# Performance work log

Measured on AMD Instinct MI355X. Metric: run time of the kernel, lower is better.

## Reference

```python
import jax, jax.numpy as jnp
import numpy as np

NEG_INF = -1e9
B, Q, M, D, H = 8, 512, 512, 1024, 16
S = D // H  # size per head


def rel_shift(x):
    # x: [B, H, Q, R] -> TransformerXL relative shift
    b, h, q, r = x.shape
    x = jnp.pad(x, ((0, 0), (0, 0), (0, 0), (1, 0)))
    x = x.reshape(b, h, r + 1, q)[:, :, 1:, :]
    return x.reshape(b, h, q, r)


def setup_inputs() -> dict:
    key = jax.random.key(0)
    ks = jax.random.split(key, 10)
    query_seqs = jax.random.normal(ks[0], (B, Q, D), jnp.float32)
    memory_seqs = jax.random.normal(ks[1], (B, M, D), jnp.float32)
    positional_encoding = jax.random.normal(ks[2], (Q + M, D), jnp.float32)
    # causal mask over concatenated [memory | query]: query token i may attend
    # to all memory tokens and query tokens <= i. 1 = masked.
    q_idx = jnp.arange(Q)[:, None]
    r_idx = jnp.arange(Q + M)[None, :]
    token_mask = (r_idx > q_idx + M).astype(jnp.float32)[None, None]  # [1,1,Q,Q+M]
    std = 0.02
    Wq = jax.random.normal(ks[3], (D, H, S), jnp.float32) * std
    Wk = jax.random.normal(ks[4], (D, H, S), jnp.float32) * std
    Wv = jax.random.normal(ks[5], (D, H, S), jnp.float32) * std
    Wr = jax.random.normal(ks[6], (D, H, S), jnp.float32) * std
    Wo = jax.random.normal(ks[7], (H, S, D), jnp.float32) * std
    content_bias = jax.random.normal(ks[8], (H, S), jnp.float32) * std
    position_bias = jax.random.normal(ks[9], (H, S), jnp.float32) * std
    return dict(query_seqs=query_seqs, memory_seqs=memory_seqs,
                positional_encoding=positional_encoding, token_mask=token_mask,
                Wq=Wq, Wk=Wk, Wv=Wv, Wr=Wr, Wo=Wo,
                content_bias=content_bias, position_bias=position_bias)


def reference(query_seqs, memory_seqs, positional_encoding, token_mask,
              Wq, Wk, Wv, Wr, Wo, content_bias, position_bias):
    # reference = [memory | query] along time axis
    reference_seqs = jnp.concatenate([memory_seqs, query_seqs], axis=1)  # [B,R,D]
    q = jnp.einsum('bqd,dhs->bqhs', query_seqs, Wq)       # [B,Q,H,S]
    k = jnp.einsum('brd,dhs->brhs', reference_seqs, Wk)   # [B,R,H,S]
    v = jnp.einsum('brd,dhs->brhs', reference_seqs, Wv)   # [B,R,H,S]
    r = jnp.einsum('rd,dhs->rhs', positional_encoding, Wr)  # [R,H,S]

    content = jnp.einsum('bqhs,brhs->bhqr', q + content_bias, k)
    positions = jnp.einsum('bqhs,rhs->bhqr', q + position_bias, r)
    positions = rel_shift(positions)

    logits = (content + positions) / jnp.sqrt(jnp.float32(S))
    logits = logits + token_mask * NEG_INF
    attn = jax.nn.softmax(logits, axis=3)  # dropout disabled (inference)

    out = jnp.einsum('bhqr,brhs->bqhs', attn, v)
    return jnp.einsum('bqhs,hsd->bqd', out, Wo)
```

## Files before the change

### kernel.cpp

```cpp
#include <hip/hip_runtime.h>

typedef _Float16 f16;
typedef _Float16 f16x8 __attribute__((ext_vector_type(8)));
typedef float f32x4 __attribute__((ext_vector_type(4)));

#define MFMA_F16(a, b, c) __builtin_amdgcn_mfma_f32_16x16x32_f16((a), (b), (c), 0, 0, 0)

#define SCL 0.125f

__device__ __forceinline__ void gl_lds16(const void* g, void* l) {
    __builtin_amdgcn_global_load_lds((const __attribute__((address_space(1))) unsigned int*)g,
                                     (__attribute__((address_space(3))) unsigned int*)l, 16, 0, 0);
}

__global__ void prep(const float* __restrict__ q, const float* __restrict__ mem,
                     const float* __restrict__ Wq, const float* __restrict__ Wk,
                     const float* __restrict__ Wv, const float* __restrict__ Wr,
                     const float* __restrict__ Wo,
                     f16* __restrict__ wt, f16* __restrict__ ref16)
{
    __shared__ float t[32][33];
    const int bid = blockIdx.x, tid = threadIdx.x;
    if (bid < 5120) {
        const int wi = bid >> 10, tt = bid & 1023;
        const float* src;
        switch (wi) { case 0: src = Wq; break; case 1: src = Wk; break;
                      case 2: src = Wv; break; case 3: src = Wr; break; default: src = Wo; }
        f16* dst = wt + ((size_t)wi << 20);
        const int x = (tt & 31) * 32, y = (tt >> 5) * 32;
        const int tx = tid & 31, ty = tid >> 5;
#pragma unroll
        for (int k2 = 0; k2 < 4; ++k2)
            t[ty + k2 * 8][tx] = src[(size_t)(y + ty + k2 * 8) * 1024 + x + tx];
        __syncthreads();
#pragma unroll
        for (int k2 = 0; k2 < 4; ++k2)
            dst[(size_t)(x + ty + k2 * 8) * 1024 + y + tx] = (f16)t[tx][ty + k2 * 8];
    } else {
        const int idx = (bid - 5120) * 256 + tid;
        const int half = idx >> 19;
        const int c = idx & 0x7FFFF;
        const int b = c >> 16, i = (c >> 7) & 511, ch = c & 127;
        const float* src = (half == 0 ? q : mem) + (((size_t)(b * 512 + i)) << 10) + ch * 8;
        const int t2 = (half == 0) ? (512 + i) : i;
        f16* dst = ref16 + ((((size_t)b << 10) + t2) << 10) + ch * 8;
        const float4 f0 = reinterpret_cast<const float4*>(src)[0];
        const float4 f1 = reinterpret_cast<const float4*>(src)[1];
        f16x8 v;
        v[0] = (f16)f0.x; v[1] = (f16)f0.y; v[2] = (f16)f0.z; v[3] = (f16)f0.w;
        v[4] = (f16)f1.x; v[5] = (f16)f1.y; v[6] = (f16)f1.z; v[7] = (f16)f1.w;
        *reinterpret_cast<f16x8*>(dst) = v;
    }
}

__global__ __launch_bounds__(512, 4)
void proj_kernel(const f16* __restrict__ ref16, const float* __restrict__ posenc,
                 const f16* __restrict__ wts,
                 f16* __restrict__ qc16, f16* __restrict__ qp16,
                 f16* __restrict__ k16, f16* __restrict__ vT16, f16* __restrict__ r16,
                 const float* __restrict__ cb, const float* __restrict__ pbias)
{
    __shared__ __align__(16) f16 SH[24576];
    f16* At = SH;
    f16* Bt = SH + 8192;

    const int tid = threadIdx.x, lane = tid & 63, w = tid >> 6;
    const int wr = w >> 2, wc = w & 3;

    const int bid = blockIdx.x;
    int mode, local, perx, shf;
    if (bid < 128)       { mode = 0; local = bid;        perx = 4; shf = 2; }
    else if (bid < 384)  { mode = 1; local = bid - 128;  perx = 8; shf = 3; }
    else if (bid < 640)  { mode = 2; local = bid - 384;  perx = 8; shf = 3; }
    else                 { mode = 3; local = bid - 640;  perx = 1; shf = 0; }
    const int xcd = local & 7, m = local >> 3;
    const int rt = xcd * perx + (m & (perx - 1));
    const int ct = m >> shf;
    const int i0 = rt * 128, n0 = ct * 256;
    const f16* BT = wts + ((size_t)mode << 20);

    f32x4 acc[4][4] = {};

    for (int ks = 0; ks < 16; ++ks) {
        const int k0 = ks * 64;
#pragma unroll
        for (int it = 0; it < 2; ++it) {
            const int c = tid + it * 512;
            const int row = c >> 3, ch = c & 7, chs = ch ^ (row & 7);
            const int grow = i0 + row;
            char* lA = reinterpret_cast<char*>(At) + ((c & ~63) << 4);
            if (mode == 3) {
                const float* sr = posenc + (size_t)grow * 1024 + k0 + ch * 8;
                const float4 f0 = reinterpret_cast<const float4*>(sr)[0];
                const float4 f1 = reinterpret_cast<const float4*>(sr)[1];
                f16x8 av;
                av[0] = (f16)f0.x; av[1] = (f16)f0.y; av[2] = (f16)f0.z; av[3] = (f16)f0.w;
                av[4] = (f16)f1.x; av[5] = (f16)f1.y; av[6] = (f16)f1.z; av[7] = (f16)f1.w;
                *reinterpret_cast<f16x8*>(reinterpret_cast<char*>(At) + row * 128 + (chs << 4)) = av;
            } else {
                const size_t arow = (mode == 0) ? (size_t)((grow >> 9) * 1024 + 512 + (grow & 511))
                                                : (size_t)grow;
                gl_lds16(ref16 + arow * 1024 + k0 + chs * 8, lA);
            }
        }
#pragma unroll
        for (int it = 0; it < 4; ++it) {
            const int c = tid + it * 512;
            const int row = c >> 3, ch = c & 7, chs = ch ^ (row & 7);
            char* lB = reinterpret_cast<char*>(Bt) + ((c & ~63) << 4);
            gl_lds16(BT + (size_t)(n0 + row) * 1024 + k0 + chs * 8, lB);
        }
        __syncthreads();
#pragma unroll
        for (int kk = 0; kk < 2; ++kk) {
            f16x8 avf[4], bvf[4];
            const int chh = kk * 4 + (lane >> 4);
#pragma unroll
            for (int mi = 0; mi < 4; ++mi) {
                const int row = wr * 64 + mi * 16 + (lane & 15);
                avf[mi] = *reinterpret_cast<const f16x8*>(reinterpret_cast<char*>(At) + row * 128 + ((chh ^ (row & 7)) << 4));
            }
#pragma unroll
            for (int n = 0; n < 4; ++n) {
                const int row = wc * 64 + n * 16 + (lane & 15);
                bvf[n] = *reinterpret_cast<const f16x8*>(reinterpret_cast<char*>(Bt) + row * 128 + ((chh ^ (row & 7)) << 4));
            }
#pragma unroll
            for (int mi = 0; mi < 4; ++mi)
#pragma unroll
                for (int n = 0; n < 4; ++n)
                    acc[mi][n] = MFMA_F16(avf[mi], bvf[n], acc[mi][n]);
        }
        __syncthreads();
    }

    if (mode == 2) {
#pragma unroll
        for (int hf = 0; hf < 2; ++hf) {
            if ((wc >> 1) == hf) {
#pragma unroll
                for (int mi = 0; mi < 4; ++mi)
#pragma unroll
                    for (int n = 0; n < 4; ++n)
#pragma unroll
                        for (int rg = 0; rg < 4; ++rg) {
                            const int jl = wr * 64 + mi * 16 + (lane >> 4) * 4 + rg;
                            const int cl = (wc & 1) * 64 + n * 16 + (lane & 15);
                            SH[cl * 128 + jl] = (f16)acc[mi][n][rg];
                        }
            }
            __syncthreads();
            const int b = i0 >> 10;
            const int j0l = i0 & 1023;
#pragma unroll
            for (int it = 0; it < 4; ++it) {
                const int c = tid + it * 512;
                const int cl = c >> 4, ch = c & 15;
                const int col = n0 + hf * 128 + cl;
                const int h = col >> 6, s = col & 63;
                f16* dst = vT16 + (((size_t)(b * 16 + h) * 64 + s) * 1024 + j0l + ch * 8);
                *reinterpret_cast<f16x8*>(dst) = *reinterpret_cast<const f16x8*>(SH + cl * 128 + ch * 8);
            }
            __syncthreads();
        }
    } else {
#pragma unroll
        for (int mi = 0; mi < 4; ++mi)
#pragma unroll
            for (int n = 0; n < 4; ++n)
#pragma unroll
                for (int rg = 0; rg < 4; ++rg) {
                    const int row = i0 + wr * 64 + mi * 16 + (lane >> 4) * 4 + rg;
                    const int col = n0 + wc * 64 + n * 16 + (lane & 15);
                    const float v = acc[mi][n][rg];
                    if (mode == 0) {
                        const int b = row >> 9, i = row & 511, h = col >> 6, s = col & 63;
                        const size_t idx = (((size_t)(b * 16 + h) * 512) + i) * 64 + s;
                        qc16[idx] = (f16)((v + cb[col]) * SCL);
                        qp16[idx] = (f16)((v + pbias[col]) * SCL);
                    } else if (mode == 1) {
                        const int b = row >> 10, j = row & 1023, h = col >> 6, s = col & 63;
                        k16[(((size_t)(b * 16 + h) * 1024) + j) * 64 + s] = (f16)v;
                    } else {
                        const int h = col >> 6, s = col & 63;
                        r16[((size_t)h * 1024 + row) * 64 + s] = (f16)v;
                    }
                }
    }
}

__global__ __launch_bounds__(512, 4)
void oproj_kernel(const f16* __restrict__ ao16, const f16* __restrict__ WoT, float* __restrict__ out)
{
    __shared__ __align__(16) f16 SH[24576];
    f16* At = SH;
    f16* Bt = SH + 8192;
    const int tid = threadIdx.x, lane = tid & 63, w = tid >> 6;
    const int wr = w >> 2, wc = w & 3;
    const int xcd = blockIdx.x & 7, m = blockIdx.x >> 3;
    const int rt = xcd * 4 + (m & 3), ct = m >> 2;
    const int i0 = rt * 128, n0 = ct * 256;

    f32x4 acc[4][4] = {};
    for (int ks = 0; ks < 16; ++ks) {
        const int k0 = ks * 64;
#pragma unroll
        for (int it = 0; it < 2; ++it) {
            const int c = tid + it * 512;
            const int row = c >> 3, ch = c & 7, chs = ch ^ (row & 7);
            gl_lds16(ao16 + (size_t)(i0 + row) * 1024 + k0 + chs * 8,
                     reinterpret_cast<char*>(At) + ((c & ~63) << 4));
        }
#pragma unroll
        for (int it = 0; it < 4; ++it) {
            const int c = tid + it * 512;
            const int row = c >> 3, ch = c & 7, chs = ch ^ (row & 7);
            gl_lds16(WoT + (size_t)(n0 + row) * 1024 + k0 + chs * 8,
                     reinterpret_cast<char*>(Bt) + ((c & ~63) << 4));
        }
        __syncthreads();
#pragma unroll
        for (int kk = 0; kk < 2; ++kk) {
            f16x8 avf[4], bvf[4];
            const int chh = kk * 4 + (lane >> 4);
#pragma unroll
            for (int mi = 0; mi < 4; ++mi) {
                const int row = wr * 64 + mi * 16 + (lane & 15);
                avf[mi] = *reinterpret_cast<const f16x8*>(reinterpret_cast<char*>(At) + row * 128 + ((chh ^ (row & 7)) << 4));
            }
#pragma unroll
            for (int n = 0; n < 4; ++n) {
                const int row = wc * 64 + n * 16 + (lane & 15);
                bvf[n] = *reinterpret_cast<const f16x8*>(reinterpret_cast<char*>(Bt) + row * 128 + ((chh ^ (row & 7)) << 4));
            }
#pragma unroll
            for (int mi = 0; mi < 4; ++mi)
#pragma unroll
                for (int n = 0; n < 4; ++n)
                    acc[mi][n] = MFMA_F16(avf[mi], bvf[n], acc[mi][n]);
        }
        __syncthreads();
    }
#pragma unroll
    for (int mi = 0; mi < 4; ++mi)
#pragma unroll
        for (int n = 0; n < 4; ++n)
#pragma unroll
            for (int rg = 0; rg < 4; ++rg) {
                const int row = i0 + wr * 64 + mi * 16 + (lane >> 4) * 4 + rg;
                const int col = n0 + wc * 64 + n * 16 + (lane & 15);
                out[(size_t)row * 1024 + col] = acc[mi][n][rg];
            }
}

__global__ __launch_bounds__(512, 4)
void attn_kernel(const f16* __restrict__ qc16, const f16* __restrict__ qp16,
                 const f16* __restrict__ k16, const f16* __restrict__ vT16,
                 const f16* __restrict__ r16, f16* __restrict__ attnout)
{
    __shared__ __align__(16) f16 KT[4096], VT[4096], RT[4096];
    __shared__ __align__(16) f16 PR[128 * 68];
    __shared__ __align__(16) f16 PB[8 * 2 * 16 * 68];

    const int tid = threadIdx.x, lane = tid & 63, w = tid >> 6;
    const int n = blockIdx.x;
    const int xcd = n & 7, m = n >> 3;
    const int h = xcd + 8 * (m >> 5);
    const int b = (m >> 2) & 7;
    const int iB = m & 3;
    const int i0 = iB * 128;
    const int bh = b * 16 + h;

    const f16* kbase = k16 + (size_t)bh * 1024 * 64;
    const f16* vbase = vT16 + (size_t)bh * 64 * 1024;
    const f16* rbase = r16 + (size_t)h * 1024 * 64;

    f16x8 qcf[2], qpf[2];
    {
        const size_t qoff = ((size_t)bh * 512 + i0 + w * 16 + (lane & 15)) * 64;
#pragma unroll
        for (int kk = 0; kk < 2; ++kk) {
            const int ch = (kk * 4 + (lane >> 4)) * 8;
            qcf[kk] = *reinterpret_cast<const f16x8*>(qc16 + qoff + ch);
            qpf[kk] = *reinterpret_cast<const f16x8*>(qp16 + qoff + ch);
        }
    }

    auto stage64 = [&](f16* dst, const f16* src, int rowstride) {
        const int row = tid >> 3, ch = tid & 7, chs = ch ^ (row & 7);
        gl_lds16(src + (size_t)row * rowstride + chs * 8,
                 reinterpret_cast<char*>(dst) + ((tid & ~63) << 4));
    };

    auto compute_pblock = [&](int bt) {
        const int slot = bt & 1;
        f32x4 pc[4] = {};
#pragma unroll
        for (int kk = 0; kk < 2; ++kk) {
            const int chh = kk * 4 + (lane >> 4);
#pragma unroll
            for (int tf = 0; tf < 4; ++tf) {
                const int brow = tf * 16 + (lane & 15);
                const f16x8 rv = *reinterpret_cast<const f16x8*>(reinterpret_cast<char*>(RT) + brow * 128 + ((chh ^ (brow & 7)) << 4));
                pc[tf] = MFMA_F16(qpf[kk], rv, pc[tf]);
            }
        }
        f16* pbw = PB + (size_t)((w * 2 + slot) * 16) * 68;
#pragma unroll
        for (int tf = 0; tf < 4; ++tf)
#pragma unroll
            for (int rg = 0; rg < 4; ++rg) {
                const int r = (lane >> 4) * 4 + rg;
                pbw[r * 68 + tf * 16 + (lane & 15)] = (f16)pc[tf][rg];
            }
    };

    {
        const int bt0 = 6 - 2 * iB;
        stage64(RT, rbase + (size_t)(bt0 * 64) * 64, 64);
        __syncthreads();
        compute_pblock(bt0);
        __syncthreads();
        stage64(RT, rbase + (size_t)((bt0 + 1) * 64) * 64, 64);
        __syncthreads();
        compute_pblock(bt0 + 1);
    }

    float mrun[4] = {-1e30f, -1e30f, -1e30f, -1e30f};
    float lrun[4] = {0.f, 0.f, 0.f, 0.f};
    f32x4 o[4] = {};

    const int njt = 2 * iB + 10;
    for (int jt = 0; jt < njt; ++jt) {
        const int j0 = jt * 64;
        const int bt = jt - 2 * iB + 8;
        __syncthreads();
        stage64(KT, kbase + (size_t)j0 * 64, 64);
        stage64(VT, vbase + j0, 1024);
        if (bt <= 15) stage64(RT, rbase + (size_t)(bt * 64) * 64, 64);
        __syncthreads();

        if (w < 4 && bt <= 15) compute_pblock(bt);

        f32x4 cfr[4] = {};
        __builtin_amdgcn_s_setprio(1);
#pragma unroll
        for (int kk = 0; kk < 2; ++kk) {
            const int chh = kk * 4 + (lane >> 4);
#pragma unroll
            for (int jf = 0; jf < 4; ++jf) {
                const int brow = jf * 16 + (lane & 15);
                const f16x8 kv = *reinterpret_cast<const f16x8*>(reinterpret_cast<char*>(KT) + brow * 128 + ((chh ^ (brow & 7)) << 4));
                cfr[jf] = MFMA_F16(qcf[kk], kv, cfr[jf]);
            }
        }
        __builtin_amdgcn_s_setprio(0);

        const int tb = j0 + 511 - i0 - w * 16;
        float lg[4][4];
#pragma unroll
        for (int jf = 0; jf < 4; ++jf)
#pragma unroll
            for (int rg = 0; rg < 4; ++rg) {
                const int il = (lane >> 4) * 4 + rg;
                const int t = tb + jf * 16 + (lane & 15) - il;
                const float pv = (float)PB[(size_t)((w * 2 + ((t >> 6) & 1)) * 16 + il) * 68 + (t & 63)];
                lg[jf][rg] = (t <= 1023) ? (cfr[jf][rg] + pv) : -1e30f;
            }

        float mx[4];
#pragma unroll
        for (int rg = 0; rg < 4; ++rg) {
            float v = fmaxf(fmaxf(lg[0][rg], lg[1][rg]), fmaxf(lg[2][rg], lg[3][rg]));
#pragma unroll
            for (int d = 1; d < 16; d <<= 1) v = fmaxf(v, __shfl_xor(v, d));
            mx[rg] = v;
        }
        const float need = fmaxf(fmaxf(mx[0] - mrun[0], mx[1] - mrun[1]),
                                 fmaxf(mx[2] - mrun[2], mx[3] - mrun[3]));
        if (__all(need <= 8.0f)) {
#pragma unroll
            for (int rg = 0; rg < 4; ++rg) {
                float rs = 0.f;
                const int il = w * 16 + (lane >> 4) * 4 + rg;
#pragma unroll
                for (int jf = 0; jf < 4; ++jf) {
                    const float p = __expf(lg[jf][rg] - mrun[rg]);
                    rs += p;
                    PR[il * 68 + jf * 16 + (lane & 15)] = (f16)p;
                }
#pragma unroll
                for (int d = 1; d < 16; d <<= 1) rs += __shfl_xor(rs, d);
                lrun[rg] += rs;
            }
        } else {
#pragma unroll
            for (int rg = 0; rg < 4; ++rg) {
                const float mnew = fmaxf(mrun[rg], mx[rg]);
                const float al = __expf(mrun[rg] - mnew);
                mrun[rg] = mnew;
                float rs = 0.f;
                const int il = w * 16 + (lane >> 4) * 4 + rg;
#pragma unroll
                for (int jf = 0; jf < 4; ++jf) {
                    const float p = __expf(lg[jf][rg] - mnew);
                    rs += p;
                    PR[il * 68 + jf * 16 + (lane & 15)] = (f16)p;
                }
#pragma unroll
                for (int d = 1; d < 16; d <<= 1) rs += __shfl_xor(rs, d);
                lrun[rg] = lrun[rg] * al + rs;
#pragma unroll
                for (int sf = 0; sf < 4; ++sf) o[sf][rg] *= al;
            }
        }

        __builtin_amdgcn_s_setprio(1);
#pragma unroll
        for (int kk = 0; kk < 2; ++kk) {
            const int chh = kk * 4 + (lane >> 4);
            const int arow = w * 16 + (lane & 15);
            const f16x8 ap = *reinterpret_cast<const f16x8*>(reinterpret_cast<char*>(PR) + arow * 136 + chh * 16);
#pragma unroll
            for (int sf = 0; sf < 4; ++sf) {
                const int brow = sf * 16 + (lane & 15);
                const f16x8 vv = *reinterpret_cast<const f16x8*>(reinterpret_cast<char*>(VT) + brow * 128 + ((chh ^ (brow & 7)) << 4));
                o[sf] = MFMA_F16(ap, vv, o[sf]);
            }
        }
        __builtin_amdgcn_s_setprio(0);

        if (w >= 4 && bt <= 15) compute_pblock(bt);
    }

#pragma unroll
    for (int sf = 0; sf < 4; ++sf)
#pragma unroll
        for (int rg = 0; rg < 4; ++rg) {
            const int il = w * 16 + (lane >> 4) * 4 + rg;
            const int row = b * 512 + i0 + il;
            const int col = h * 64 + sf * 16 + (lane & 15);
            attnout[(size_t)row * 1024 + col] = (f16)(o[sf][rg] / lrun[rg]);
        }
}

extern "C" void kernel_launch(void* const* d_in, const int* in_sizes, int n_in,
                              void* d_out, int out_size, void* d_ws, size_t ws_size,
                              hipStream_t stream)
{
    const float* query = (const float*)d_in[0];
    const float* memory = (const float*)d_in[1];
    const float* posenc = (const float*)d_in[2];
    const float* Wq = (const float*)d_in[4];
    const float* Wk = (const float*)d_in[5];
    const float* Wv = (const float*)d_in[6];
    const float* Wr = (const float*)d_in[7];
    const float* Wo = (const float*)d_in[8];
    const float* cb = (const float*)d_in[9];
    const float* pb = (const float*)d_in[10];
    float* out = (float*)d_out;

    if (ws_size < (size_t)38 * (1u << 20) * sizeof(f16)) return;
    f16* ws = (f16*)d_ws;
    f16* WoT = ws + (4u << 20);
    f16* ref16 = ws + (5u << 20);
    f16* ao16 = ref16;
    f16* qc16 = ref16 + (8u << 20);
    f16* qp16 = qc16 + (4u << 20);
    f16* k16 = qp16 + (4u << 20);
    f16* vT16 = k16 + (8u << 20);
    f16* r16 = vT16 + (8u << 20);

    prep<<<9216, 256, 0, stream>>>(query, memory, Wq, Wk, Wv, Wr, Wo, ws, ref16);
    proj_kernel<<<672, 512, 0, stream>>>(ref16, posenc, ws, qc16, qp16, k16, vT16, r16, cb, pb);
    attn_kernel<<<512, 512, 0, stream>>>(qc16, qp16, k16, vT16, r16, ao16);
    oproj_kernel<<<128, 512, 0, stream>>>(ao16, WoT, out);
}
```

Measured before the change: 193.1 us.

## Triple-buffer LDS tiles with async prefetch in projection GEMM kernels

Replaces the load-sync-compute-sync loop in proj_kernel (non-posenc modes) and oproj_kernel with a three-slot LDS ring. Each K-step prefetches two steps ahead via global_load_lds, gated by explicit vmcnt waits and one barrier per step, with the prefetch split across the two inner MFMA sub-steps. The goal is to hide global-memory latency behind MFMA work and drop one barrier per iteration. In exchange LDS per block triples to 144 KB and launch bounds drop to 2 blocks per CU, which lowers occupancy.

```diff
diff --git a/kernel.cpp b/kernel.cpp
--- a/kernel.cpp
+++ b/kernel.cpp
@@ -7,6 +7,9 @@
 #define MFMA_F16(a, b, c) __builtin_amdgcn_mfma_f32_16x16x32_f16((a), (b), (c), 0, 0, 0)
 
 #define SCL 0.125f
+
+#define VM_WAIT6 asm volatile("s_waitcnt vmcnt(6)" ::: "memory")
+#define VM_WAIT0 asm volatile("s_waitcnt vmcnt(0)" ::: "memory")
 
 __device__ __forceinline__ void gl_lds16(const void* g, void* l) {
     __builtin_amdgcn_global_load_lds((const __attribute__((address_space(1))) unsigned int*)g,
@@ -53,16 +56,14 @@
     }
 }
 
-__global__ __launch_bounds__(512, 4)
+__global__ __launch_bounds__(512, 2)
 void proj_kernel(const f16* __restrict__ ref16, const float* __restrict__ posenc,
                  const f16* __restrict__ wts,
                  f16* __restrict__ qc16, f16* __restrict__ qp16,
                  f16* __restrict__ k16, f16* __restrict__ vT16, f16* __restrict__ r16,
                  const float* __restrict__ cb, const float* __restrict__ pbias)
 {
-    __shared__ __align__(16) f16 SH[24576];
-    f16* At = SH;
-    f16* Bt = SH + 8192;
+    __shared__ __align__(16) f16 SH[3 * 24576];
 
     const int tid = threadIdx.x, lane = tid & 63, w = tid >> 6;
     const int wr = w >> 2, wc = w & 3;
@@ -81,60 +82,121 @@
 
     f32x4 acc[4][4] = {};
 
-    for (int ks = 0; ks < 16; ++ks) {
+    auto stage_part = [&](int ks, int slot, int part) {
         const int k0 = ks * 64;
-#pragma unroll
-        for (int it = 0; it < 2; ++it) {
-            const int c = tid + it * 512;
+        f16* At = SH + slot * 24576;
+        f16* Bt = At + 8192;
+        if (part == 0) {
+#pragma unroll
+            for (int it = 0; it < 2; ++it) {
+                const int c = tid + it * 512;
+                const int row = c >> 3, ch = c & 7, chs = ch ^ (row & 7);
+                const int grow = i0 + row;
+                const size_t arow = (mode == 0) ? (size_t)((grow >> 9) * 1024 + 512 + (grow & 511))
+                                                : (size_t)grow;
+                gl_lds16(ref16 + arow * 1024 + k0 + chs * 8,
+                         reinterpret_cast<char*>(At) + ((c & ~63) << 4));
+            }
+            const int c = tid;
             const int row = c >> 3, ch = c & 7, chs = ch ^ (row & 7);
-            const int grow = i0 + row;
-            char* lA = reinterpret_cast<char*>(At) + ((c & ~63) << 4);
-            if (mode == 3) {
-                const float* sr = posenc + (size_t)grow * 1024 + k0 + ch * 8;
+            gl_lds16(BT + (size_t)(n0 + row) * 1024 + k0 + chs * 8,
+                     reinterpret_cast<char*>(Bt) + ((c & ~63) << 4));
+        } else {
+#pragma unroll
+            for (int it = 1; it < 4; ++it) {
+                const int c = tid + it * 512;
+                const int row = c >> 3, ch = c & 7, chs = ch ^ (row & 7);
+                gl_lds16(BT + (size_t)(n0 + row) * 1024 + k0 + chs * 8,
+                         reinterpret_cast<char*>(Bt) + ((c & ~63) << 4));
+            }
+        }
+    };
+
+    if (mode != 3) {
+        stage_part(0, 0, 0); stage_part(0, 0, 1);
+        stage_part(1, 1, 0); stage_part(1, 1, 1);
+        for (int ks = 0; ks < 16; ++ks) {
+            const int cur = ks % 3;
+            const int s2 = (ks + 2) % 3;
+            f16* At = SH + cur * 24576;
+            f16* Bt = At + 8192;
+            if (ks < 15) { VM_WAIT6; } else { VM_WAIT0; }
+            __builtin_amdgcn_sched_barrier(0);
+            __builtin_amdgcn_s_barrier();
+#pragma unroll
+            for (int kk = 0; kk < 2; ++kk) {
+                f16x8 avf[4], bvf[4];
+                const int chh = kk * 4 + (lane >> 4);
+#pragma unroll
+                for (int mi = 0; mi < 4; ++mi) {
+                    const int row = wr * 64 + mi * 16 + (lane & 15);
+                    avf[mi] = *reinterpret_cast<const f16x8*>(reinterpret_cast<char*>(At) + row * 128 + ((chh ^ (row & 7)) << 4));
+                }
+#pragma unroll
+                for (int n = 0; n < 4; ++n) {
+                    const int row = wc * 64 + n * 16 + (lane & 15);
+                    bvf[n] = *reinterpret_cast<const f16x8*>(reinterpret_cast<char*>(Bt) + row * 128 + ((chh ^ (row & 7)) << 4));
+                }
+                if (ks < 14) stage_part(ks + 2, s2, kk);
+#pragma unroll
+                for (int mi = 0; mi < 4; ++mi)
+#pragma unroll
+                    for (int n = 0; n < 4; ++n)
+                        acc[mi][n] = MFMA_F16(avf[mi], bvf[n], acc[mi][n]);
+                __builtin_amdgcn_sched_barrier(0);
+            }
+        }
+    } else {
+        f16* At = SH;
+        f16* Bt = SH + 8192;
+        for (int ks = 0; ks < 16; ++ks) {
+            const int k0 = ks * 64;
+#pragma unroll
+            for (int it = 0; it < 2; ++it) {
+                const int c = tid + it * 512;
+                const int row = c >> 3, ch = c & 7, chs = ch ^ (row & 7);
+                const float* sr = posenc + (size_t)(i0 + row) * 1024 + k0 + ch * 8;
                 const float4 f0 = reinterpret_cast<const float4*>(sr)[0];
                 const float4 f1 = reinterpret_cast<const float4*>(sr)[1];
                 f16x8 av;
                 av[0] = (f16)f0.x; av[1] = (f16)f0.y; av[2] = (f16)f0.z; av[3] = (f16)f0.w;
                 av[4] = (f16)f1.x; av[5] = (f16)f1.y; av[6] = (f16)f1.z; av[7] = (f16)f1.w;
                 *reinterpret_cast<f16x8*>(reinterpret_cast<char*>(At) + row * 128 + (chs << 4)) = av;
-            } else {
-                const size_t arow = (mode == 0) ? (size_t)((grow >> 9) * 1024 + 512 + (grow & 511))
-                                                : (size_t)grow;
-                gl_lds16(ref16 + arow * 1024 + k0 + chs * 8, lA);
-            }
-        }
-#pragma unroll
-        for (int it = 0; it < 4; ++it) {
-            const int c = tid + it * 512;
-            const int row = c >> 3, ch = c & 7, chs = ch ^ (row & 7);
-            char* lB = reinterpret_cast<char*>(Bt) + ((c & ~63) << 4);
-            gl_lds16(BT + (size_t)(n0 + row) * 1024 + k0 + chs * 8, lB);
-        }
-        __syncthreads();
-#pragma unroll
-        for (int kk = 0; kk < 2; ++kk) {
-            f16x8 avf[4], bvf[4];
-            const int chh = kk * 4 + (lane >> 4);
-#pragma unroll
-            for (int mi = 0; mi < 4; ++mi) {
-                const int row = wr * 64 + mi * 16 + (lane & 15);
-                avf[mi] = *reinterpret_cast<const f16x8*>(reinterpret_cast<char*>(At) + row * 128 + ((chh ^ (row & 7)) << 4));
-            }
-#pragma unroll
-            for (int n = 0; n < 4; ++n) {
-                const int row = wc * 64 + n * 16 + (lane & 15);
-                bvf[n] = *reinterpret_cast<const f16x8*>(reinterpret_cast<char*>(Bt) + row * 128 + ((chh ^ (row & 7)) << 4));
-            }
-#pragma unroll
-            for (int mi = 0; mi < 4; ++mi)
-#pragma unroll
-                for (int n = 0; n < 4; ++n)
-                    acc[mi][n] = MFMA_F16(avf[mi], bvf[n], acc[mi][n]);
-        }
-        __syncthreads();
+            }
+#pragma unroll
+            for (int it = 0; it < 4; ++it) {
+                const int c = tid + it * 512;
+                const int row = c >> 3, ch = c & 7, chs = ch ^ (row & 7);
+                gl_lds16(BT + (size_t)(n0 + row) * 1024 + k0 + chs * 8,
+                         reinterpret_cast<char*>(Bt) + ((c & ~63) << 4));
+            }
+            __syncthreads();
+#pragma unroll
+            for (int kk = 0; kk < 2; ++kk) {
+                f16x8 avf[4], bvf[4];
+                const int chh = kk * 4 + (lane >> 4);
+#pragma unroll
+                for (int mi = 0; mi < 4; ++mi) {
+                    const int row = wr * 64 + mi * 16 + (lane & 15);
+                    avf[mi] = *reinterpret_cast<const f16x8*>(reinterpret_cast<char*>(At) + row * 128 + ((chh ^ (row & 7)) << 4));
+                }
+#pragma unroll
+                for (int n = 0; n < 4; ++n) {
+                    const int row = wc * 64 + n * 16 + (lane & 15);
+                    bvf[n] = *reinterpret_cast<const f16x8*>(reinterpret_cast<char*>(Bt) + row * 128 + ((chh ^ (row & 7)) << 4));
+                }
+#pragma unroll
+                for (int mi = 0; mi < 4; ++mi)
+#pragma unroll
+                    for (int n = 0; n < 4; ++n)
+                        acc[mi][n] = MFMA_F16(avf[mi], bvf[n], acc[mi][n]);
+            }
+            __syncthreads();
+        }
     }
 
     if (mode == 2) {
+        __syncthreads();
 #pragma unroll
         for (int hf = 0; hf < 2; ++hf) {
             if ((wc >> 1) == hf) {
@@ -189,12 +251,10 @@
     }
 }
 
-__global__ __launch_bounds__(512, 4)
+__global__ __launch_bounds__(512, 2)
 void oproj_kernel(const f16* __restrict__ ao16, const f16* __restrict__ WoT, float* __restrict__ out)
 {
-    __shared__ __align__(16) f16 SH[24576];
-    f16* At = SH;
-    f16* Bt = SH + 8192;
+    __shared__ __align__(16) f16 SH[3 * 24576];
     const int tid = threadIdx.x, lane = tid & 63, w = tid >> 6;
     const int wr = w >> 2, wc = w & 3;
     const int xcd = blockIdx.x & 7, m = blockIdx.x >> 3;
@@ -202,23 +262,44 @@
     const int i0 = rt * 128, n0 = ct * 256;
 
     f32x4 acc[4][4] = {};
-    for (int ks = 0; ks < 16; ++ks) {
+
+    auto stage_part = [&](int ks, int slot, int part) {
         const int k0 = ks * 64;
-#pragma unroll
-        for (int it = 0; it < 2; ++it) {
-            const int c = tid + it * 512;
-            const int row = c >> 3, ch = c & 7, chs = ch ^ (row & 7);
-            gl_lds16(ao16 + (size_t)(i0 + row) * 1024 + k0 + chs * 8,
-                     reinterpret_cast<char*>(At) + ((c & ~63) << 4));
-        }
-#pragma unroll
-        for (int it = 0; it < 4; ++it) {
-            const int c = tid + it * 512;
+        f16* At = SH + slot * 24576;
+        f16* Bt = At + 8192;
+        if (part == 0) {
+#pragma unroll
+            for (int it = 0; it < 2; ++it) {
+                const int c = tid + it * 512;
+                const int row = c >> 3, ch = c & 7, chs = ch ^ (row & 7);
+                gl_lds16(ao16 + (size_t)(i0 + row) * 1024 + k0 + chs * 8,
+                         reinterpret_cast<char*>(At) + ((c & ~63) << 4));
+            }
+            const int c = tid;
             const int row = c >> 3, ch = c & 7, chs = ch ^ (row & 7);
             gl_lds16(WoT + (size_t)(n0 + row) * 1024 + k0 + chs * 8,
                      reinterpret_cast<char*>(Bt) + ((c & ~63) << 4));
-        }
-        __syncthreads();
+        } else {
+#pragma unroll
+            for (int it = 1; it < 4; ++it) {
+                const int c = tid + it * 512;
+                const int row = c >> 3, ch = c & 7, chs = ch ^ (row & 7);
+                gl_lds16(WoT + (size_t)(n0 + row) * 1024 + k0 + chs * 8,
+                         reinterpret_cast<char*>(Bt) + ((c & ~63) << 4));
+            }
+        }
+    };
+
+    stage_part(0, 0, 0); stage_part(0, 0, 1);
+    stage_part(1, 1, 0); stage_part(1, 1, 1);
+    for (int ks = 0; ks < 16; ++ks) {
+        const int cur = ks % 3;
+        const int s2 = (ks + 2) % 3;
+        f16* At = SH + cur * 24576;
+        f16* Bt = At + 8192;
+        if (ks < 15) { VM_WAIT6; } else { VM_WAIT0; }
+        __builtin_amdgcn_sched_barrier(0);
+        __builtin_amdgcn_s_barrier();
 #pragma unroll
         for (int kk = 0; kk < 2; ++kk) {
             f16x8 avf[4], bvf[4];
@@ -233,14 +314,16 @@
                 const int row = wc * 64 + n * 16 + (lane & 15);
                 bvf[n] = *reinterpret_cast<const f16x8*>(reinterpret_cast<char*>(Bt) + row * 128 + ((chh ^ (row & 7)) << 4));
             }
+            if (ks < 14) stage_part(ks + 2, s2, kk);
 #pragma unroll
             for (int mi = 0; mi < 4; ++mi)
 #pragma unroll
                 for (int n = 0; n < 4; ++n)
                     acc[mi][n] = MFMA_F16(avf[mi], bvf[n], acc[mi][n]);
-        }
-        __syncthreads();
-    }
+            __builtin_amdgcn_sched_barrier(0);
+        }
+    }
+
 #pragma unroll
     for (int mi = 0; mi < 4; ++mi)
 #pragma unroll
```

Result: faster. 183.5 us (-5.0%).

## Fuse K and V projections to share the reference-sequence A tile

Applied to the files above, without the earlier changes.

The projection kernel now computes the K and V projections in one block. The block loads the reference activation tile once and multiplies it against both the Wk and Wv tiles, keeping two accumulator sets. This removes duplicate A-tile loads and cuts the grid from 672 to 416 blocks. In exchange it doubles accumulator registers and grows LDS use (launch bounds drop to 2 blocks per CU), which lowers occupancy, and the K/V blocks become heavier than the Q and R blocks, which may hurt load balance.

```diff
diff --git a/kernel.cpp b/kernel.cpp
--- a/kernel.cpp
+++ b/kernel.cpp
@@ -53,33 +53,35 @@
     }
 }
 
-__global__ __launch_bounds__(512, 4)
+__global__ __launch_bounds__(512, 2)
 void proj_kernel(const f16* __restrict__ ref16, const float* __restrict__ posenc,
                  const f16* __restrict__ wts,
                  f16* __restrict__ qc16, f16* __restrict__ qp16,
                  f16* __restrict__ k16, f16* __restrict__ vT16, f16* __restrict__ r16,
                  const float* __restrict__ cb, const float* __restrict__ pbias)
 {
-    __shared__ __align__(16) f16 SH[24576];
+    __shared__ __align__(16) f16 SH[40960];
     f16* At = SH;
-    f16* Bt = SH + 8192;
+    f16* Bk = SH + 8192;
+    f16* Bv = SH + 24576;
 
     const int tid = threadIdx.x, lane = tid & 63, w = tid >> 6;
     const int wr = w >> 2, wc = w & 3;
 
     const int bid = blockIdx.x;
     int mode, local, perx, shf;
-    if (bid < 128)       { mode = 0; local = bid;        perx = 4; shf = 2; }
-    else if (bid < 384)  { mode = 1; local = bid - 128;  perx = 8; shf = 3; }
-    else if (bid < 640)  { mode = 2; local = bid - 384;  perx = 8; shf = 3; }
-    else                 { mode = 3; local = bid - 640;  perx = 1; shf = 0; }
+    if (bid < 256)      { mode = 0; local = bid;       perx = 8; shf = 3; }
+    else if (bid < 384) { mode = 1; local = bid - 256; perx = 4; shf = 2; }
+    else                { mode = 2; local = bid - 384; perx = 1; shf = 0; }
     const int xcd = local & 7, m = local >> 3;
     const int rt = xcd * perx + (m & (perx - 1));
     const int ct = m >> shf;
     const int i0 = rt * 128, n0 = ct * 256;
-    const f16* BT = wts + ((size_t)mode << 20);
-
-    f32x4 acc[4][4] = {};
+    const f16* BT0 = (mode == 0) ? wts + (1u << 20) : (mode == 1) ? wts : wts + (3u << 20);
+    const f16* BTv = wts + (2u << 20);
+
+    f32x4 acck[4][4] = {};
+    f32x4 accv[4][4] = {};
 
     for (int ks = 0; ks < 16; ++ks) {
         const int k0 = ks * 64;
@@ -88,8 +90,7 @@
             const int c = tid + it * 512;
             const int row = c >> 3, ch = c & 7, chs = ch ^ (row & 7);
             const int grow = i0 + row;
-            char* lA = reinterpret_cast<char*>(At) + ((c & ~63) << 4);
-            if (mode == 3) {
+            if (mode == 2) {
                 const float* sr = posenc + (size_t)grow * 1024 + k0 + ch * 8;
                 const float4 f0 = reinterpret_cast<const float4*>(sr)[0];
                 const float4 f1 = reinterpret_cast<const float4*>(sr)[1];
@@ -98,22 +99,32 @@
                 av[4] = (f16)f1.x; av[5] = (f16)f1.y; av[6] = (f16)f1.z; av[7] = (f16)f1.w;
                 *reinterpret_cast<f16x8*>(reinterpret_cast<char*>(At) + row * 128 + (chs << 4)) = av;
             } else {
-                const size_t arow = (mode == 0) ? (size_t)((grow >> 9) * 1024 + 512 + (grow & 511))
+                const size_t arow = (mode == 1) ? (size_t)((grow >> 9) * 1024 + 512 + (grow & 511))
                                                 : (size_t)grow;
-                gl_lds16(ref16 + arow * 1024 + k0 + chs * 8, lA);
+                gl_lds16(ref16 + arow * 1024 + k0 + chs * 8,
+                         reinterpret_cast<char*>(At) + ((c & ~63) << 4));
             }
         }
 #pragma unroll
         for (int it = 0; it < 4; ++it) {
             const int c = tid + it * 512;
             const int row = c >> 3, ch = c & 7, chs = ch ^ (row & 7);
-            char* lB = reinterpret_cast<char*>(Bt) + ((c & ~63) << 4);
-            gl_lds16(BT + (size_t)(n0 + row) * 1024 + k0 + chs * 8, lB);
+            gl_lds16(BT0 + (size_t)(n0 + row) * 1024 + k0 + chs * 8,
+                     reinterpret_cast<char*>(Bk) + ((c & ~63) << 4));
+        }
+        if (mode == 0) {
+#pragma unroll
+            for (int it = 0; it < 4; ++it) {
+                const int c = tid + it * 512;
+                const int row = c >> 3, ch = c & 7, chs = ch ^ (row & 7);
+                gl_lds16(BTv + (size_t)(n0 + row) * 1024 + k0 + chs * 8,
+                         reinterpret_cast<char*>(Bv) + ((c & ~63) << 4));
+            }
         }
         __syncthreads();
 #pragma unroll
         for (int kk = 0; kk < 2; ++kk) {
-            f16x8 avf[4], bvf[4];
+            f16x8 avf[4], bkf[4];
             const int chh = kk * 4 + (lane >> 4);
 #pragma unroll
             for (int mi = 0; mi < 4; ++mi) {
@@ -123,18 +134,44 @@
 #pragma unroll
             for (int n = 0; n < 4; ++n) {
                 const int row = wc * 64 + n * 16 + (lane & 15);
-                bvf[n] = *reinterpret_cast<const f16x8*>(reinterpret_cast<char*>(Bt) + row * 128 + ((chh ^ (row & 7)) << 4));
+                bkf[n] = *reinterpret_cast<const f16x8*>(reinterpret_cast<char*>(Bk) + row * 128 + ((chh ^ (row & 7)) << 4));
             }
 #pragma unroll
             for (int mi = 0; mi < 4; ++mi)
 #pragma unroll
                 for (int n = 0; n < 4; ++n)
-                    acc[mi][n] = MFMA_F16(avf[mi], bvf[n], acc[mi][n]);
-        }
-        __syncthreads();
-    }
-
-    if (mode == 2) {
+                    acck[mi][n] = MFMA_F16(avf[mi], bkf[n], acck[mi][n]);
+            if (mode == 0) {
+                f16x8 bvf[4];
+#pragma unroll
+                for (int n = 0; n < 4; ++n) {
+                    const int row = wc * 64 + n * 16 + (lane & 15);
+                    bvf[n] = *reinterpret_cast<const f16x8*>(reinterpret_cast<char*>(Bv) + row * 128 + ((chh ^ (row & 7)) << 4));
+                }
+#pragma unroll
+                for (int mi = 0; mi < 4; ++mi)
+#pragma unroll
+                    for (int n = 0; n < 4; ++n)
+                        accv[mi][n] = MFMA_F16(avf[mi], bvf[n], accv[mi][n]);
+            }
+        }
+        __syncthreads();
+    }
+
+    if (mode == 0) {
+#pragma unroll
+        for (int mi = 0; mi < 4; ++mi)
+#pragma unroll
+            for (int n = 0; n < 4; ++n)
+#pragma unroll
+                for (int rg = 0; rg < 4; ++rg) {
+                    const int row = i0 + wr * 64 + mi * 16 + (lane >> 4) * 4 + rg;
+                    const int col = n0 + wc * 64 + n * 16 + (lane & 15);
+                    const int b = row >> 10, j = row & 1023, h = col >> 6, s = col & 63;
+                    k16[(((size_t)(b * 16 + h) * 1024) + j) * 64 + s] = (f16)acck[mi][n][rg];
+                }
+        const int b = i0 >> 10;
+        const int j0l = i0 & 1023;
 #pragma unroll
         for (int hf = 0; hf < 2; ++hf) {
             if ((wc >> 1) == hf) {
@@ -146,12 +183,10 @@
                         for (int rg = 0; rg < 4; ++rg) {
                             const int jl = wr * 64 + mi * 16 + (lane >> 4) * 4 + rg;
                             const int cl = (wc & 1) * 64 + n * 16 + (lane & 15);
-                            SH[cl * 128 + jl] = (f16)acc[mi][n][rg];
+                            SH[cl * 128 + jl] = (f16)accv[mi][n][rg];
                         }
             }
             __syncthreads();
-            const int b = i0 >> 10;
-            const int j0l = i0 & 1023;
 #pragma unroll
             for (int it = 0; it < 4; ++it) {
                 const int c = tid + it * 512;
@@ -172,15 +207,12 @@
                 for (int rg = 0; rg < 4; ++rg) {
                     const int row = i0 + wr * 64 + mi * 16 + (lane >> 4) * 4 + rg;
                     const int col = n0 + wc * 64 + n * 16 + (lane & 15);
-                    const float v = acc[mi][n][rg];
-                    if (mode == 0) {
+                    const float v = acck[mi][n][rg];
+                    if (mode == 1) {
                         const int b = row >> 9, i = row & 511, h = col >> 6, s = col & 63;
                         const size_t idx = (((size_t)(b * 16 + h) * 512) + i) * 64 + s;
                         qc16[idx] = (f16)((v + cb[col]) * SCL);
                         qp16[idx] = (f16)((v + pbias[col]) * SCL);
-                    } else if (mode == 1) {
-                        const int b = row >> 10, j = row & 1023, h = col >> 6, s = col & 63;
-                        k16[(((size_t)(b * 16 + h) * 1024) + j) * 64 + s] = (f16)v;
                     } else {
                         const int h = col >> 6, s = col & 63;
                         r16[((size_t)h * 1024 + row) * 64 + s] = (f16)v;
@@ -472,7 +504,7 @@
     f16* r16 = vT16 + (8u << 20);
 
     prep<<<9216, 256, 0, stream>>>(query, memory, Wq, Wk, Wv, Wr, Wo, ws, ref16);
-    proj_kernel<<<672, 512, 0, stream>>>(ref16, posenc, ws, qc16, qp16, k16, vT16, r16, cb, pb);
+    proj_kernel<<<416, 512, 0, stream>>>(ref16, posenc, ws, qc16, qp16, k16, vT16, r16, cb, pb);
     attn_kernel<<<512, 512, 0, stream>>>(qc16, qp16, k16, vT16, r16, ao16);
     oproj_kernel<<<128, 512, 0, stream>>>(ao16, WoT, out);
 }
```

After: 196.6 us. No clear change (+1.8%).
